# Performance work log

Hardware: AMD Instinct MI355X
Metric: run time of the kernel (lower is better)

## Reference

```python
import jax, jax.numpy as jnp
import numpy as np

U, I, D = 60000, 90000, 64
N = U + I
NNZ_R, NNZ_S = 1_000_000, 1_000_000
N_RATINGS = 5
RATING_LAYERS = 2
SOCIAL_LAYERS = 2
EMB_COMB = 1.0


def setup_inputs() -> dict:
    key = jax.random.key(0)
    ks = jax.random.split(key, 24)
    inp = {
        'rating_rows': jax.random.randint(ks[0], (N_RATINGS, NNZ_R), 0, N, dtype=jnp.int32),
        'rating_cols': jax.random.randint(ks[1], (N_RATINGS, NNZ_R), 0, N, dtype=jnp.int32),
        'rating_vals': jax.random.uniform(ks[2], (N_RATINGS, NNZ_R), dtype=jnp.float32),
        'friend_rows': jax.random.randint(ks[3], (NNZ_S,), 0, U, dtype=jnp.int32),
        'friend_cols': jax.random.randint(ks[4], (NNZ_S,), 0, U, dtype=jnp.int32),
        'friend_vals': jax.random.uniform(ks[5], (NNZ_S,), dtype=jnp.float32),
        'group_rows': jax.random.randint(ks[6], (NNZ_S,), 0, U, dtype=jnp.int32),
        'group_cols': jax.random.randint(ks[7], (NNZ_S,), 0, U, dtype=jnp.int32),
        'group_vals': jax.random.uniform(ks[8], (NNZ_S,), dtype=jnp.float32),
        'rating_user_emb': jax.random.normal(ks[9], (N_RATINGS, U, D), dtype=jnp.float32) * 0.1,
        'rating_item_emb': jax.random.normal(ks[10], (N_RATINGS, I, D), dtype=jnp.float32) * 0.1,
        'friend_emb': jax.random.normal(ks[11], (U, D), dtype=jnp.float32) * 0.1,
        'group_emb': jax.random.normal(ks[12], (U, D), dtype=jnp.float32) * 0.1,
        'user_att_w': jax.random.normal(ks[13], (D,), dtype=jnp.float32) * 0.1,
        'user_att_mat_w': jax.random.normal(ks[14], (D, D), dtype=jnp.float32) * 0.1,
        'item_att_w': jax.random.normal(ks[15], (D,), dtype=jnp.float32) * 0.1,
        'item_att_mat_w': jax.random.normal(ks[16], (D, D), dtype=jnp.float32) * 0.1,
        'social_att_w': jax.random.normal(ks[17], (D,), dtype=jnp.float32) * 0.1,
        'social_att_mat_w': jax.random.normal(ks[18], (D, D), dtype=jnp.float32) * 0.1,
        'adaptive_emb_comb': jax.random.uniform(ks[19], (U,), dtype=jnp.float32) + 0.5,
    }
    return inp


def _spmm(rows, cols, vals, x, n):
    # COO sparse matmul: out[r] += vals[e] * x[cols[e]]
    return jax.ops.segment_sum(vals[:, None] * x[cols], rows, num_segments=n)


def _l2norm(x):
    # F.normalize(x, p=2, dim=1)
    return x / jnp.clip(jnp.linalg.norm(x, axis=1, keepdims=True), 1e-12)


def _att_fuse(embs, a, M):
    # embs: [C, N, D]; weight[c,n] = tanh((emb @ M.T) @ a); softmax over channels C
    w = jnp.tanh(jnp.einsum('cnd,ed,e->cn', embs, M, a))
    scores = jax.nn.softmax(w, axis=0)  # [C, N]
    mixed = jnp.einsum('cn,cnd->nd', scores, embs)
    return mixed, scores


def reference(rating_rows, rating_cols, rating_vals,
              friend_rows, friend_cols, friend_vals,
              group_rows, group_cols, group_vals,
              rating_user_emb, rating_item_emb, friend_emb, group_emb,
              user_att_w, user_att_mat_w, item_att_w, item_att_mat_w,
              social_att_w, social_att_mat_w, adaptive_emb_comb):
    # ---- rating channels: LightGCN propagation over bipartite graph ----
    user_list, item_list = [], []
    for c in range(N_RATINGS):
        ego = jnp.concatenate([rating_user_emb[c], rating_item_emb[c]], axis=0)  # [N, D]
        layers = []
        for _ in range(RATING_LAYERS):
            ego = _spmm(rating_rows[c], rating_cols[c], rating_vals[c], ego, N)
            layers.append(ego)
        mean_emb = jnp.mean(jnp.stack(layers, axis=0), axis=0)
        user_list.append(mean_emb[:U])
        item_list.append(mean_emb[U:])
    user_embs = jnp.stack(user_list, axis=0)  # [C, U, D]
    item_embs = jnp.stack(item_list, axis=0)  # [C, I, D]
    mixed_rating_user, user_scores = _att_fuse(user_embs, user_att_w, user_att_mat_w)
    mixed_rating_item, item_scores = _att_fuse(item_embs, item_att_w, item_att_mat_w)

    # ---- social channels: propagation + per-layer L2 normalize ----
    def social_prop(rows, cols, vals, emb):
        outs = []
        for _ in range(SOCIAL_LAYERS):
            emb = _l2norm(_spmm(rows, cols, vals, emb, U))
            outs.append(emb)
        return jnp.mean(jnp.stack(outs, axis=0), axis=0)

    friend_u = social_prop(friend_rows, friend_cols, friend_vals, friend_emb)
    group_u = social_prop(group_rows, group_cols, group_vals, group_emb)
    social_embs = jnp.stack([friend_u, group_u], axis=0)  # [2, U, D]
    mixed_social, social_scores = _att_fuse(social_embs, social_att_w, social_att_mat_w)

    # ---- adaptive combination ----
    num = jnp.sum(mixed_rating_user * mixed_social, axis=1)
    denom = (jnp.clip(jnp.linalg.norm(mixed_rating_user, axis=1), 1e-8)
             * jnp.clip(jnp.linalg.norm(mixed_social, axis=1), 1e-8))
    emb_sim = num / denom
    emb_sim_up_0 = jnp.maximum(emb_sim, 0.0)
    base = (SOCIAL_LAYERS + RATING_LAYERS) / 2.0
    rate = EMB_COMB / (base + emb_sim_up_0 * adaptive_emb_comb)[:, None]  # [U, 1]
    mixed_user = mixed_rating_user + mixed_social * rate
    return (user_scores, item_scores, social_scores, mixed_user, mixed_rating_item)
```

## Files before the change

### kernel.cpp

```cpp
#include <hip/hip_runtime.h>
#include <hip/hip_bf16.h>

#define UU 60000
#define II 90000
#define DD 64
#define NN 150000
#define NNZC 1000000
#define NTOT 7000000
#define MTOT 870000
#define ROW_S0 750000
#define NBR 733
#define NBCK 1046
#define CAPE 8192
#define ACH 16384
#define GRID_A 428
#define ABLK 1024

__device__ __forceinline__ int wave_incl_scan(int x) {
    int lane = threadIdx.x & 63;
#pragma unroll
    for (int d = 1; d < 64; d <<= 1) {
        int y = __shfl_up(x, d, 64);
        if (lane >= d) x += y;
    }
    return x;
}

__device__ int block_incl_scan(int x, int* lds) {
    int wid = threadIdx.x >> 6, lane = threadIdx.x & 63;
    int ws_ = wave_incl_scan(x);
    if (lane == 63) lds[wid] = ws_;
    __syncthreads();
    int off = 0;
    for (int w = 0; w < wid; ++w) off += lds[w];
    __syncthreads();
    return ws_ + off;
}

__device__ __forceinline__ float2 unpack_bf16x2(unsigned p) {
    float2 r;
    r.x = __uint_as_float(p << 16);
    r.y = __uint_as_float(p & 0xffff0000u);
    return r;
}

__device__ __forceinline__ unsigned pack_bf16x2(float a, float b) {
    __hip_bfloat162 h = __float22bfloat162_rn(make_float2(a, b));
    return *(unsigned*)&h;
}

__device__ __forceinline__ uint2 pack4(float4 m) {
    return make_uint2(pack_bf16x2(m.x, m.y), pack_bf16x2(m.z, m.w));
}

__device__ __forceinline__ float4 unpack4(uint2 p) {
    float2 a = unpack_bf16x2(p.x), b = unpack_bf16x2(p.y);
    return make_float4(a.x, a.y, b.x, b.y);
}

__device__ __forceinline__ int bid_of(int grow) {
    return (grow < ROW_S0) ? (grow >> 10) : NBR + (grow - ROW_S0) / 384;
}

__global__ void att_vec_kernel(const float* __restrict__ au, const float* __restrict__ Mu,
                               const float* __restrict__ ai, const float* __restrict__ Mi,
                               const float* __restrict__ as_, const float* __restrict__ Ms,
                               float* __restrict__ v) {
    int d = threadIdx.x;
    float su = 0.f, si = 0.f, ss = 0.f;
    for (int e = 0; e < DD; ++e) {
        su += au[e] * Mu[e * DD + d];
        si += ai[e] * Mi[e * DD + d];
        ss += as_[e] * Ms[e * DD + d];
    }
    v[d] = su;
    v[DD + d] = si;
    v[2 * DD + d] = ss;
}

__device__ __forceinline__ void decode_full(int e, const int* __restrict__ rR,
                                            const int* __restrict__ rC, const float* __restrict__ rV,
                                            const int* __restrict__ fR, const int* __restrict__ fC,
                                            const float* __restrict__ fV,
                                            const int* __restrict__ gR, const int* __restrict__ gC,
                                            const float* __restrict__ gV,
                                            int& grow, int& c, float& v) {
    if (e < 5 * NNZC) { grow = (e / NNZC) * NN + rR[e]; c = rC[e]; v = rV[e]; }
    else if (e < 6 * NNZC) { int k = e - 5 * NNZC; grow = ROW_S0 + fR[k]; c = fC[k]; v = fV[k]; }
    else { int k = e - 6 * NNZC; grow = ROW_S0 + UU + gR[k]; c = gC[k]; v = gV[k]; }
}

__global__ __launch_bounds__(ABLK) void pa_count_kernel(const int* __restrict__ rR,
                                                        const int* __restrict__ fR,
                                                        const int* __restrict__ gR,
                                                        int* __restrict__ gHistT) {
    __shared__ int lcnt[NBCK];
    int k = blockIdx.x;
    int cbase = k * ACH;
    int eEnd = min(cbase + ACH, NTOT);
    for (int b = threadIdx.x; b < NBCK; b += ABLK) lcnt[b] = 0;
    __syncthreads();
    for (int e0 = cbase + threadIdx.x; e0 < eEnd; e0 += 4 * ABLK) {
        int gw[4]; bool val[4];
#pragma unroll
        for (int u = 0; u < 4; ++u) {
            int e = e0 + u * ABLK;
            val[u] = e < eEnd;
            int ec = val[u] ? e : cbase;
            if (ec < 5 * NNZC) gw[u] = (ec / NNZC) * NN + rR[ec];
            else if (ec < 6 * NNZC) gw[u] = ROW_S0 + fR[ec - 5 * NNZC];
            else gw[u] = ROW_S0 + UU + gR[ec - 6 * NNZC];
        }
#pragma unroll
        for (int u = 0; u < 4; ++u)
            if (val[u]) atomicAdd(&lcnt[bid_of(gw[u])], 1);
    }
    __syncthreads();
    for (int b = threadIdx.x; b < NBCK; b += ABLK)
        gHistT[(size_t)b * GRID_A + k] = lcnt[b];
}

__global__ void kprefix_kernel(int* __restrict__ gHistT, int* __restrict__ bTot) {
    int b = blockIdx.x * (blockDim.x >> 6) + (threadIdx.x >> 6);
    if (b >= NBCK) return;
    int lane = threadIdx.x & 63;
    int* g = gHistT + (size_t)b * GRID_A;
    int carry = 0;
    for (int c0 = 0; c0 < GRID_A; c0 += 64) {
        int idx = c0 + lane;
        int v = (idx < GRID_A) ? g[idx] : 0;
        int incl = wave_incl_scan(v);
        if (idx < GRID_A) g[idx] = carry + incl - v;
        carry += __shfl(incl, 63, 64);
    }
    if (lane == 0) bTot[b] = carry;
}

__global__ void bscan_kernel(const int* __restrict__ bTot, int* __restrict__ bStart,
                             int* __restrict__ rowptr) {
    __shared__ int lds8[8];
    __shared__ int sOff;
    if (threadIdx.x == 0) sOff = 0;
    __syncthreads();
    for (int base = 0; base < NBCK; base += 256) {
        int i = base + threadIdx.x;
        int v = (i < NBCK) ? bTot[i] : 0;
        int incl = block_incl_scan(v, lds8);
        if (i < NBCK) bStart[i] = sOff + incl - v;
        __syncthreads();
        if (threadIdx.x == 255) sOff += incl;
        __syncthreads();
    }
    if (threadIdx.x == 0) { bStart[NBCK] = sOff; rowptr[MTOT] = sOff; }
}

__global__ __launch_bounds__(ABLK) void pa_scatter_kernel(
        const int* __restrict__ rR, const int* __restrict__ rC, const float* __restrict__ rV,
        const int* __restrict__ fR, const int* __restrict__ fC, const float* __restrict__ fV,
        const int* __restrict__ gR, const int* __restrict__ gC, const float* __restrict__ gV,
        const int* __restrict__ bStart, const int* __restrict__ gHistT,
        uint2* __restrict__ ecv) {
    __shared__ int lcur[NBCK];
    int k = blockIdx.x;
    int cbase = k * ACH;
    int eEnd = min(cbase + ACH, NTOT);
    for (int b = threadIdx.x; b < NBCK; b += ABLK)
        lcur[b] = bStart[b] + gHistT[(size_t)b * GRID_A + k];
    __syncthreads();
    for (int e0 = cbase + threadIdx.x; e0 < eEnd; e0 += 4 * ABLK) {
        int gw[4], cc[4]; float vv[4]; bool val[4];
#pragma unroll
        for (int u = 0; u < 4; ++u) {
            int e = e0 + u * ABLK;
            val[u] = e < eEnd;
            int ec = val[u] ? e : cbase;
            decode_full(ec, rR, rC, rV, fR, fC, fV, gR, gC, gV, gw[u], cc[u], vv[u]);
        }
        int pos[4];
#pragma unroll
        for (int u = 0; u < 4; ++u)
            pos[u] = val[u] ? atomicAdd(&lcur[bid_of(gw[u])], 1) : 0;
#pragma unroll
        for (int u = 0; u < 4; ++u) {
            if (!val[u]) continue;
            int lrow = (gw[u] < ROW_S0) ? (gw[u] & 1023) : ((gw[u] - ROW_S0) % 384);
            ecv[pos[u]] = make_uint2(((unsigned)lrow << 18) | (unsigned)cc[u],
                                     __float_as_uint(vv[u]));
        }
    }
}

__global__ __launch_bounds__(256) void phaseB_kernel(const int* __restrict__ bStart,
                                                     int* __restrict__ rowptr,
                                                     const uint2* __restrict__ ecv,
                                                     uint2* __restrict__ edata) {
    __shared__ unsigned short perm[CAPE];
    __shared__ int off[1024];
    __shared__ int lds8[8];
    int b = blockIdx.x;
    int firstRow = (b < NBR) ? (b << 10) : ROW_S0 + (b - NBR) * 384;
    int rowEnd = (b < NBR) ? min((b + 1) << 10, ROW_S0)
                           : min(ROW_S0 + (b - NBR + 1) * 384, MTOT);
    int nRows = rowEnd - firstRow;
    int dst = bStart[b];
    int count = bStart[b + 1] - dst;
    for (int i = threadIdx.x; i < nRows; i += 256) off[i] = 0;
    __syncthreads();
    for (int i = threadIdx.x; i < count; i += 256)
        atomicAdd(&off[ecv[dst + i].x >> 18], 1);
    __syncthreads();
    int base4 = threadIdx.x * 4;
    int v4[4], s = 0;
#pragma unroll
    for (int kk = 0; kk < 4; ++kk) {
        int i = base4 + kk;
        v4[kk] = (i < nRows) ? off[i] : 0;
        s += v4[kk];
    }
    int incl = block_incl_scan(s, lds8);
    int run = incl - s;
#pragma unroll
    for (int kk = 0; kk < 4; ++kk) {
        int i = base4 + kk;
        if (i < nRows) { rowptr[firstRow + i] = dst + run; off[i] = run; }
        run += v4[kk];
    }
    __syncthreads();
    if (count <= CAPE) {
        for (int i = threadIdx.x; i < count; i += 256) {
            int pos = atomicAdd(&off[ecv[dst + i].x >> 18], 1);
            perm[pos] = (unsigned short)i;
        }
        __syncthreads();
        for (int i = threadIdx.x; i < count; i += 256) {
            uint2 e = ecv[dst + perm[i]];
            edata[dst + i] = make_uint2(e.x & 0x3FFFFu, e.y);
        }
    } else {
        for (int i = threadIdx.x; i < count; i += 256) {
            uint2 e = ecv[dst + i];
            int pos = atomicAdd(&off[e.x >> 18], 1);
            edata[dst + pos] = make_uint2(e.x & 0x3FFFFu, e.y);
        }
    }
}

template <int MODE>
__global__ __launch_bounds__(256) void spmm_kernel(
        const int* __restrict__ rowptr, int rowBase,
        const uint2* __restrict__ edata,
        const float* __restrict__ xloF, const float* __restrict__ xhiF,
        const uint2* __restrict__ tblB,
        const uint2* __restrict__ selfB, const float* __restrict__ vvec,
        uint2* __restrict__ outB, float4* __restrict__ outF,
        float* __restrict__ wOut, int nRows) {
    int lane = threadIdx.x & 63;
    int l16 = lane & 15;
    int grpBase = lane & 48;
    int wid = blockIdx.x * (blockDim.x >> 6) + (threadIdx.x >> 6);
    int row = wid * 4 + (lane >> 4);
    bool active = row < nRows;
    int g = rowBase + row;
    int start = active ? rowptr[g] : 0;
    int end = active ? rowptr[g + 1] : 0;
    float4 acc = make_float4(0.f, 0.f, 0.f, 0.f);
    for (int j0 = start; j0 < end; j0 += 16) {
        uint2 md = make_uint2(0u, 0u);
        if (j0 + l16 < end) md = edata[j0 + l16];
        int cnt = min(end - j0, 16);
        for (int js = 0; js < cnt; js += 8) {
            int cc[8]; float vv[8]; float4 xv[8];
#pragma unroll
            for (int u = 0; u < 8; ++u) {
                int jj = js + u;
                int sl = grpBase + ((jj < cnt) ? jj : 0);
                cc[u] = __shfl((int)md.x, sl, 64);
                float v = __uint_as_float((unsigned)__shfl((int)md.y, sl, 64));
                vv[u] = (jj < cnt) ? v : 0.f;
            }
#pragma unroll
            for (int u = 0; u < 8; ++u) {
                int c = cc[u];
                if (MODE == 0) {
                    const float* src = (c < UU) ? (xloF + (size_t)c * DD)
                                                : (xhiF + (size_t)(c - UU) * DD);
                    xv[u] = *(const float4*)(src + 4 * l16);
                } else if (MODE == 2) {
                    xv[u] = *(const float4*)(xloF + (size_t)c * DD + 4 * l16);
                } else {
                    xv[u] = unpack4(tblB[(size_t)c * 16 + l16]);
                }
            }
#pragma unroll
            for (int u = 0; u < 8; ++u) {
                acc.x += vv[u] * xv[u].x; acc.y += vv[u] * xv[u].y;
                acc.z += vv[u] * xv[u].z; acc.w += vv[u] * xv[u].w;
            }
        }
    }
    if (!active) return;
    size_t ro = (size_t)row * 16 + l16;
    if (MODE == 0) {
        outB[ro] = pack4(acc);
    } else if (MODE == 1) {
        float4 sv = unpack4(selfB[ro]);
        float4 m = make_float4(0.5f * (acc.x + sv.x), 0.5f * (acc.y + sv.y),
                               0.5f * (acc.z + sv.z), 0.5f * (acc.w + sv.w));
        outB[ro] = pack4(m);
        const float* vv = (row < UU) ? vvec : (vvec + DD);
        float4 vw = *(const float4*)(vv + 4 * l16);
        float p = m.x * vw.x + m.y * vw.y + m.z * vw.z + m.w * vw.w;
        p += __shfl_xor(p, 1, 64); p += __shfl_xor(p, 2, 64);
        p += __shfl_xor(p, 4, 64); p += __shfl_xor(p, 8, 64);
        if (l16 == 0) wOut[row] = tanhf(p);
    } else if (MODE == 2) {
        float n2 = acc.x * acc.x + acc.y * acc.y + acc.z * acc.z + acc.w * acc.w;
        n2 += __shfl_xor(n2, 1, 64); n2 += __shfl_xor(n2, 2, 64);
        n2 += __shfl_xor(n2, 4, 64); n2 += __shfl_xor(n2, 8, 64);
        float inv = 1.f / fmaxf(sqrtf(n2), 1e-12f);
        outB[ro] = pack4(make_float4(acc.x * inv, acc.y * inv, acc.z * inv, acc.w * inv));
    } else {
        float n2 = acc.x * acc.x + acc.y * acc.y + acc.z * acc.z + acc.w * acc.w;
        n2 += __shfl_xor(n2, 1, 64); n2 += __shfl_xor(n2, 2, 64);
        n2 += __shfl_xor(n2, 4, 64); n2 += __shfl_xor(n2, 8, 64);
        float inv = 1.f / fmaxf(sqrtf(n2), 1e-12f);
        float4 sv = unpack4(selfB[ro]);
        outF[ro] = make_float4(0.5f * (sv.x + acc.x * inv), 0.5f * (sv.y + acc.y * inv),
                               0.5f * (sv.z + acc.z * inv), 0.5f * (sv.w + acc.w * inv));
    }
}

__global__ void mix5_kernel(const __hip_bfloat16* __restrict__ chanEmb,
                            const float* __restrict__ w,
                            float* __restrict__ oUS, float* __restrict__ oIS,
                            float* __restrict__ mixedRU, float* __restrict__ oMI) {
    int lane = threadIdx.x & 63;
    int n = blockIdx.x * (blockDim.x >> 6) + (threadIdx.x >> 6);
    if (n >= NN) return;
    float sw[5];
    float mx = -2.0f;
#pragma unroll
    for (int c = 0; c < 5; ++c) {
        sw[c] = w[(size_t)c * NN + n];
        mx = fmaxf(mx, sw[c]);
    }
    float sum = 0.f;
#pragma unroll
    for (int c = 0; c < 5; ++c) {
        sw[c] = expf(sw[c] - mx);
        sum += sw[c];
    }
    float inv = 1.0f / sum;
    float acc = 0.f;
#pragma unroll
    for (int c = 0; c < 5; ++c) {
        sw[c] *= inv;
        acc += sw[c] * __bfloat162float(chanEmb[((size_t)c * NN + n) * DD + lane]);
    }
    if (n < UU) {
#pragma unroll
        for (int c = 0; c < 5; ++c)
            if (lane == c) oUS[(size_t)c * UU + n] = sw[c];
        mixedRU[(size_t)n * DD + lane] = acc;
    } else {
        int m = n - UU;
#pragma unroll
        for (int c = 0; c < 5; ++c)
            if (lane == c) oIS[(size_t)c * II + m] = sw[c];
        oMI[(size_t)m * DD + lane] = acc;
    }
}

__global__ void social_mix_final_kernel(const float* __restrict__ e0, const float* __restrict__ e1,
                                        const float* __restrict__ vs,
                                        const float* __restrict__ mixedRU,
                                        const float* __restrict__ adaptive,
                                        float* __restrict__ scoresOut,
                                        float* __restrict__ outMU) {
    int lane = threadIdx.x & 63;
    int n = blockIdx.x * (blockDim.x >> 6) + (threadIdx.x >> 6);
    if (n >= UU) return;
    size_t idx = (size_t)n * DD + lane;
    float a = e0[idx];
    float b = e1[idx];
    float v = vs[lane];
    float pa = a * v, pb = b * v;
    float mru = mixedRU[idx];
#pragma unroll
    for (int m = 32; m >= 1; m >>= 1) { pa += __shfl_xor(pa, m, 64); pb += __shfl_xor(pb, m, 64); }
    float w0 = tanhf(pa);
    float w1 = tanhf(pb);
    float mx = fmaxf(w0, w1);
    float x0 = expf(w0 - mx);
    float x1 = expf(w1 - mx);
    float invs = 1.0f / (x0 + x1);
    float s0 = x0 * invs;
    float s1 = x1 * invs;
    if (lane == 0) {
        scoresOut[n] = s0;
        scoresOut[UU + n] = s1;
    }
    float ms = s0 * a + s1 * b;
    float nm = mru * ms, na2 = mru * mru, nb2 = ms * ms;
#pragma unroll
    for (int m = 32; m >= 1; m >>= 1) {
        nm += __shfl_xor(nm, m, 64); na2 += __shfl_xor(na2, m, 64); nb2 += __shfl_xor(nb2, m, 64);
    }
    float denom = fmaxf(sqrtf(na2), 1e-8f) * fmaxf(sqrtf(nb2), 1e-8f);
    float sim = nm / denom;
    float rate = 1.0f / (2.0f + fmaxf(sim, 0.f) * adaptive[n]);
    outMU[idx] = mru + ms * rate;
}

extern "C" void kernel_launch(void* const* d_in, const int* in_sizes, int n_in,
                              void* d_out, int out_size, void* d_ws, size_t ws_size,
                              hipStream_t stream) {
    const int* r_rows = (const int*)d_in[0];
    const int* r_cols = (const int*)d_in[1];
    const float* r_vals = (const float*)d_in[2];
    const int* f_rows = (const int*)d_in[3];
    const int* f_cols = (const int*)d_in[4];
    const float* f_vals = (const float*)d_in[5];
    const int* g_rows = (const int*)d_in[6];
    const int* g_cols = (const int*)d_in[7];
    const float* g_vals = (const float*)d_in[8];
    const float* rue = (const float*)d_in[9];
    const float* rie = (const float*)d_in[10];
    const float* femb = (const float*)d_in[11];
    const float* gemb = (const float*)d_in[12];
    const float* uaw = (const float*)d_in[13];
    const float* uamw = (const float*)d_in[14];
    const float* iaw = (const float*)d_in[15];
    const float* iamw = (const float*)d_in[16];
    const float* saw = (const float*)d_in[17];
    const float* samw = (const float*)d_in[18];
    const float* adapt = (const float*)d_in[19];

    float* ws = (float*)d_ws;
    size_t o = 0;
    int* rowptr = (int*)(ws + o); o += 870016;
    int* bStart = (int*)(ws + o); o += 2048;
    int* bTot   = (int*)(ws + o); o += 2048;
    int* gHistT = (int*)(ws + o); o += 448000;
    float* R1 = ws + o; o += 14000000;
    float* edF = ws + o; o += 14000000;
    float* R2 = ws + o; o += 24000000;
    float* wrat = ws + o; o += 750016;
    float* vvec = ws + o; o += 192;

    uint2* ecv = (uint2*)R1;
    uint2* edata = (uint2*)edF;
    uint2* AtmpB = (uint2*)R1;
    float* mixedRU = R1;
    float* socM0 = R1 + 4800000;
    float* socM1 = R1 + 8640000;
    __hip_bfloat16* chanMean = (__hip_bfloat16*)R2;
    uint2* socL1B = (uint2*)R2;

    float* out = (float*)d_out;
    float* oUS = out;
    float* oIS = oUS + (size_t)5 * UU;
    float* oSS = oIS + (size_t)5 * II;
    float* oMU = oSS + (size_t)2 * UU;
    float* oMI = oMU + (size_t)UU * DD;

    const dim3 blk(256);
    const dim3 blkA(ABLK);
    const int gridN4 = (NN + 15) / 16;
    const int gridU4 = (UU + 15) / 16;
    const int gridMix = (NN + 3) / 4;
    const int gridFin = (UU + 3) / 4;

    att_vec_kernel<<<1, 64, 0, stream>>>(uaw, uamw, iaw, iamw, saw, samw, vvec);

    pa_count_kernel<<<GRID_A, blkA, 0, stream>>>(r_rows, f_rows, g_rows, gHistT);
    kprefix_kernel<<<(NBCK + 3) / 4, blk, 0, stream>>>(gHistT, bTot);
    bscan_kernel<<<1, blk, 0, stream>>>(bTot, bStart, rowptr);
    pa_scatter_kernel<<<GRID_A, blkA, 0, stream>>>(r_rows, r_cols, r_vals,
                                                   f_rows, f_cols, f_vals,
                                                   g_rows, g_cols, g_vals,
                                                   bStart, gHistT, ecv);
    phaseB_kernel<<<NBCK, blk, 0, stream>>>(bStart, rowptr, ecv, edata);

    for (int c = 0; c < 5; ++c) {
        spmm_kernel<0><<<gridN4, blk, 0, stream>>>(
            rowptr, c * NN, edata,
            rue + (size_t)c * UU * DD, rie + (size_t)c * II * DD, nullptr,
            nullptr, nullptr, AtmpB, nullptr, nullptr, NN);
        spmm_kernel<1><<<gridN4, blk, 0, stream>>>(
            rowptr, c * NN, edata,
            nullptr, nullptr, AtmpB, AtmpB, vvec,
            (uint2*)(chanMean + (size_t)c * NN * DD), nullptr, wrat + (size_t)c * NN, NN);
    }

    mix5_kernel<<<gridMix, blk, 0, stream>>>(chanMean, wrat, oUS, oIS, mixedRU, oMI);

    spmm_kernel<2><<<gridU4, blk, 0, stream>>>(rowptr, ROW_S0, edata, femb, nullptr, nullptr,
                                               nullptr, nullptr, socL1B, nullptr, nullptr, UU);
    spmm_kernel<3><<<gridU4, blk, 0, stream>>>(rowptr, ROW_S0, edata, nullptr, nullptr, socL1B,
                                               socL1B, nullptr, nullptr, (float4*)socM0, nullptr, UU);
    spmm_kernel<2><<<gridU4, blk, 0, stream>>>(rowptr, ROW_S0 + UU, edata, gemb, nullptr, nullptr,
                                               nullptr, nullptr, socL1B, nullptr, nullptr, UU);
    spmm_kernel<3><<<gridU4, blk, 0, stream>>>(rowptr, ROW_S0 + UU, edata, nullptr, nullptr, socL1B,
                                               socL1B, nullptr, nullptr, (float4*)socM1, nullptr, UU);

    social_mix_final_kernel<<<gridFin, blk, 0, stream>>>(socM0, socM1, vvec + 2 * DD,
                                                         mixedRU, adapt, oSS, oMU);
}
```

Before: 662.6 us.

## Merge independent SpMM stages into combined launches and precompute scatter ranks

Layer-1 SpMM for channel c now runs in the same launch as layer-2 for channel c-1, with double-buffered intermediates. The first social layers for friend and group are fused into the rating mix kernel, and both second social layers share one launch. The count pass also records each edge's LDS atomic rank, so the scatter pass computes positions without repeating the atomics. This cuts the launch count and raises occupancy for the small kernels. In exchange it adds an extra rank array write and read, larger workspace buffers, and a runtime mode switch in the dual kernel.

```diff
diff --git a/kernel.cpp b/kernel.cpp
--- a/kernel.cpp
+++ b/kernel.cpp
@@ -16,6 +16,19 @@
 #define GRID_A 428
 #define ABLK 1024
 
+struct SpmmJob {
+    int mode;
+    int rowBase;
+    int nRows;
+    const float* xloF;
+    const float* xhiF;
+    const uint2* tblB;
+    const uint2* selfB;
+    uint2* outB;
+    float4* outF;
+    float* wOut;
+};
+
 __device__ __forceinline__ int wave_incl_scan(int x) {
     int lane = threadIdx.x & 63;
 #pragma unroll
@@ -93,7 +106,8 @@
 __global__ __launch_bounds__(ABLK) void pa_count_kernel(const int* __restrict__ rR,
                                                         const int* __restrict__ fR,
                                                         const int* __restrict__ gR,
-                                                        int* __restrict__ gHistT) {
+                                                        int* __restrict__ gHistT,
+                                                        unsigned short* __restrict__ grank) {
     __shared__ int lcnt[NBCK];
     int k = blockIdx.x;
     int cbase = k * ACH;
@@ -111,9 +125,13 @@
             else if (ec < 6 * NNZC) gw[u] = ROW_S0 + fR[ec - 5 * NNZC];
             else gw[u] = ROW_S0 + UU + gR[ec - 6 * NNZC];
         }
+        int rk[4];
 #pragma unroll
         for (int u = 0; u < 4; ++u)
-            if (val[u]) atomicAdd(&lcnt[bid_of(gw[u])], 1);
+            rk[u] = val[u] ? atomicAdd(&lcnt[bid_of(gw[u])], 1) : 0;
+#pragma unroll
+        for (int u = 0; u < 4; ++u)
+            if (val[u]) grank[e0 + u * ABLK] = (unsigned short)rk[u];
     }
     __syncthreads();
     for (int b = threadIdx.x; b < NBCK; b += ABLK)
@@ -159,7 +177,7 @@
         const int* __restrict__ fR, const int* __restrict__ fC, const float* __restrict__ fV,
         const int* __restrict__ gR, const int* __restrict__ gC, const float* __restrict__ gV,
         const int* __restrict__ bStart, const int* __restrict__ gHistT,
-        uint2* __restrict__ ecv) {
+        const unsigned short* __restrict__ grank, uint2* __restrict__ ecv) {
     __shared__ int lcur[NBCK];
     int k = blockIdx.x;
     int cbase = k * ACH;
@@ -168,24 +186,22 @@
         lcur[b] = bStart[b] + gHistT[(size_t)b * GRID_A + k];
     __syncthreads();
     for (int e0 = cbase + threadIdx.x; e0 < eEnd; e0 += 4 * ABLK) {
-        int gw[4], cc[4]; float vv[4]; bool val[4];
+        int gw[4], cc[4]; float vv[4]; int rk[4]; bool val[4];
 #pragma unroll
         for (int u = 0; u < 4; ++u) {
             int e = e0 + u * ABLK;
             val[u] = e < eEnd;
             int ec = val[u] ? e : cbase;
             decode_full(ec, rR, rC, rV, fR, fC, fV, gR, gC, gV, gw[u], cc[u], vv[u]);
-        }
-        int pos[4];
-#pragma unroll
-        for (int u = 0; u < 4; ++u)
-            pos[u] = val[u] ? atomicAdd(&lcur[bid_of(gw[u])], 1) : 0;
+            rk[u] = grank[ec];
+        }
 #pragma unroll
         for (int u = 0; u < 4; ++u) {
             if (!val[u]) continue;
+            int pos = lcur[bid_of(gw[u])] + rk[u];
             int lrow = (gw[u] < ROW_S0) ? (gw[u] & 1023) : ((gw[u] - ROW_S0) % 384);
-            ecv[pos[u]] = make_uint2(((unsigned)lrow << 18) | (unsigned)cc[u],
-                                     __float_as_uint(vv[u]));
+            ecv[pos] = make_uint2(((unsigned)lrow << 18) | (unsigned)cc[u],
+                                  __float_as_uint(vv[u]));
         }
     }
 }
@@ -246,21 +262,17 @@
 }
 
 template <int MODE>
-__global__ __launch_bounds__(256) void spmm_kernel(
-        const int* __restrict__ rowptr, int rowBase,
-        const uint2* __restrict__ edata,
-        const float* __restrict__ xloF, const float* __restrict__ xhiF,
-        const uint2* __restrict__ tblB,
-        const uint2* __restrict__ selfB, const float* __restrict__ vvec,
-        uint2* __restrict__ outB, float4* __restrict__ outF,
-        float* __restrict__ wOut, int nRows) {
+__device__ __forceinline__ void spmm_body(int blk, const SpmmJob& j,
+                                          const int* __restrict__ rowptr,
+                                          const uint2* __restrict__ edata,
+                                          const float* __restrict__ vvec) {
     int lane = threadIdx.x & 63;
     int l16 = lane & 15;
     int grpBase = lane & 48;
-    int wid = blockIdx.x * (blockDim.x >> 6) + (threadIdx.x >> 6);
+    int wid = blk * (int)(blockDim.x >> 6) + (threadIdx.x >> 6);
     int row = wid * 4 + (lane >> 4);
-    bool active = row < nRows;
-    int g = rowBase + row;
+    bool active = row < j.nRows;
+    int g = j.rowBase + row;
     int start = active ? rowptr[g] : 0;
     int end = active ? rowptr[g + 1] : 0;
     float4 acc = make_float4(0.f, 0.f, 0.f, 0.f);
@@ -282,13 +294,13 @@
             for (int u = 0; u < 8; ++u) {
                 int c = cc[u];
                 if (MODE == 0) {
-                    const float* src = (c < UU) ? (xloF + (size_t)c * DD)
-                                                : (xhiF + (size_t)(c - UU) * DD);
+                    const float* src = (c < UU) ? (j.xloF + (size_t)c * DD)
+                                                : (j.xhiF + (size_t)(c - UU) * DD);
                     xv[u] = *(const float4*)(src + 4 * l16);
                 } else if (MODE == 2) {
-                    xv[u] = *(const float4*)(xloF + (size_t)c * DD + 4 * l16);
+                    xv[u] = *(const float4*)(j.xloF + (size_t)c * DD + 4 * l16);
                 } else {
-                    xv[u] = unpack4(tblB[(size_t)c * 16 + l16]);
+                    xv[u] = unpack4(j.tblB[(size_t)c * 16 + l16]);
                 }
             }
 #pragma unroll
@@ -301,41 +313,73 @@
     if (!active) return;
     size_t ro = (size_t)row * 16 + l16;
     if (MODE == 0) {
-        outB[ro] = pack4(acc);
+        j.outB[ro] = pack4(acc);
     } else if (MODE == 1) {
-        float4 sv = unpack4(selfB[ro]);
+        float4 sv = unpack4(j.selfB[ro]);
         float4 m = make_float4(0.5f * (acc.x + sv.x), 0.5f * (acc.y + sv.y),
                                0.5f * (acc.z + sv.z), 0.5f * (acc.w + sv.w));
-        outB[ro] = pack4(m);
+        j.outB[ro] = pack4(m);
         const float* vv = (row < UU) ? vvec : (vvec + DD);
         float4 vw = *(const float4*)(vv + 4 * l16);
         float p = m.x * vw.x + m.y * vw.y + m.z * vw.z + m.w * vw.w;
         p += __shfl_xor(p, 1, 64); p += __shfl_xor(p, 2, 64);
         p += __shfl_xor(p, 4, 64); p += __shfl_xor(p, 8, 64);
-        if (l16 == 0) wOut[row] = tanhf(p);
+        if (l16 == 0) j.wOut[row] = tanhf(p);
     } else if (MODE == 2) {
         float n2 = acc.x * acc.x + acc.y * acc.y + acc.z * acc.z + acc.w * acc.w;
         n2 += __shfl_xor(n2, 1, 64); n2 += __shfl_xor(n2, 2, 64);
         n2 += __shfl_xor(n2, 4, 64); n2 += __shfl_xor(n2, 8, 64);
         float inv = 1.f / fmaxf(sqrtf(n2), 1e-12f);
-        outB[ro] = pack4(make_float4(acc.x * inv, acc.y * inv, acc.z * inv, acc.w * inv));
+        j.outB[ro] = pack4(make_float4(acc.x * inv, acc.y * inv, acc.z * inv, acc.w * inv));
     } else {
         float n2 = acc.x * acc.x + acc.y * acc.y + acc.z * acc.z + acc.w * acc.w;
         n2 += __shfl_xor(n2, 1, 64); n2 += __shfl_xor(n2, 2, 64);
         n2 += __shfl_xor(n2, 4, 64); n2 += __shfl_xor(n2, 8, 64);
         float inv = 1.f / fmaxf(sqrtf(n2), 1e-12f);
-        float4 sv = unpack4(selfB[ro]);
-        outF[ro] = make_float4(0.5f * (sv.x + acc.x * inv), 0.5f * (sv.y + acc.y * inv),
-                               0.5f * (sv.z + acc.z * inv), 0.5f * (sv.w + acc.w * inv));
-    }
-}
-
-__global__ void mix5_kernel(const __hip_bfloat16* __restrict__ chanEmb,
-                            const float* __restrict__ w,
-                            float* __restrict__ oUS, float* __restrict__ oIS,
-                            float* __restrict__ mixedRU, float* __restrict__ oMI) {
+        float4 sv = unpack4(j.selfB[ro]);
+        j.outF[ro] = make_float4(0.5f * (sv.x + acc.x * inv), 0.5f * (sv.y + acc.y * inv),
+                                 0.5f * (sv.z + acc.z * inv), 0.5f * (sv.w + acc.w * inv));
+    }
+}
+
+template <int MODE>
+__global__ __launch_bounds__(256) void spmm_kernel(SpmmJob j, const int* __restrict__ rowptr,
+                                                   const uint2* __restrict__ edata,
+                                                   const float* __restrict__ vvec) {
+    spmm_body<MODE>(blockIdx.x, j, rowptr, edata, vvec);
+}
+
+__global__ __launch_bounds__(256) void spmm_dual_kernel(SpmmJob a, int aBlocks, SpmmJob b,
+                                                        const int* __restrict__ rowptr,
+                                                        const uint2* __restrict__ edata,
+                                                        const float* __restrict__ vvec) {
+    SpmmJob j;
+    int blk;
+    if ((int)blockIdx.x < aBlocks) { j = a; blk = blockIdx.x; }
+    else { j = b; blk = blockIdx.x - aBlocks; }
+    switch (j.mode) {
+        case 0: spmm_body<0>(blk, j, rowptr, edata, vvec); break;
+        case 1: spmm_body<1>(blk, j, rowptr, edata, vvec); break;
+        case 2: spmm_body<2>(blk, j, rowptr, edata, vvec); break;
+        default: spmm_body<3>(blk, j, rowptr, edata, vvec); break;
+    }
+}
+
+__global__ __launch_bounds__(256) void mix_social_kernel(
+        const __hip_bfloat16* __restrict__ chanEmb, const float* __restrict__ w,
+        float* __restrict__ oUS, float* __restrict__ oIS,
+        float* __restrict__ mixedRU, float* __restrict__ oMI, int nMix,
+        SpmmJob s0, int s0Blocks, SpmmJob s1,
+        const int* __restrict__ rowptr, const uint2* __restrict__ edata,
+        const float* __restrict__ vvec) {
+    if ((int)blockIdx.x >= nMix) {
+        int r = blockIdx.x - nMix;
+        if (r < s0Blocks) spmm_body<2>(r, s0, rowptr, edata, vvec);
+        else spmm_body<2>(r - s0Blocks, s1, rowptr, edata, vvec);
+        return;
+    }
     int lane = threadIdx.x & 63;
-    int n = blockIdx.x * (blockDim.x >> 6) + (threadIdx.x >> 6);
+    int n = blockIdx.x * 4 + (threadIdx.x >> 6);
     if (n >= NN) return;
     float sw[5];
     float mx = -2.0f;
@@ -369,6 +413,14 @@
             if (lane == c) oIS[(size_t)c * II + m] = sw[c];
         oMI[(size_t)m * DD + lane] = acc;
     }
+}
+
+__global__ __launch_bounds__(256) void social2_kernel(SpmmJob s0, int s0Blocks, SpmmJob s1,
+                                                      const int* __restrict__ rowptr,
+                                                      const uint2* __restrict__ edata,
+                                                      const float* __restrict__ vvec) {
+    if ((int)blockIdx.x < s0Blocks) spmm_body<3>(blockIdx.x, s0, rowptr, edata, vvec);
+    else spmm_body<3>(blockIdx.x - s0Blocks, s1, rowptr, edata, vvec);
 }
 
 __global__ void social_mix_final_kernel(const float* __restrict__ e0, const float* __restrict__ e1,
@@ -447,15 +499,19 @@
     float* R2 = ws + o; o += 24000000;
     float* wrat = ws + o; o += 750016;
     float* vvec = ws + o; o += 192;
+    float* socF = ws + o; o += 3840000;
 
     uint2* ecv = (uint2*)R1;
     uint2* edata = (uint2*)edF;
-    uint2* AtmpB = (uint2*)R1;
+    unsigned short* grank = (unsigned short*)R2;
+    uint2* AtmpB0 = (uint2*)R1;
+    uint2* AtmpB1 = AtmpB0 + (size_t)NN * 16;
     float* mixedRU = R1;
     float* socM0 = R1 + 4800000;
     float* socM1 = R1 + 8640000;
     __hip_bfloat16* chanMean = (__hip_bfloat16*)R2;
-    uint2* socL1B = (uint2*)R2;
+    uint2* socL1B0 = (uint2*)socF;
+    uint2* socL1B1 = socL1B0 + (size_t)UU * 16;
 
     float* out = (float*)d_out;
     float* oUS = out;
@@ -473,36 +529,51 @@
 
     att_vec_kernel<<<1, 64, 0, stream>>>(uaw, uamw, iaw, iamw, saw, samw, vvec);
 
-    pa_count_kernel<<<GRID_A, blkA, 0, stream>>>(r_rows, f_rows, g_rows, gHistT);
+    pa_count_kernel<<<GRID_A, blkA, 0, stream>>>(r_rows, f_rows, g_rows, gHistT, grank);
     kprefix_kernel<<<(NBCK + 3) / 4, blk, 0, stream>>>(gHistT, bTot);
     bscan_kernel<<<1, blk, 0, stream>>>(bTot, bStart, rowptr);
     pa_scatter_kernel<<<GRID_A, blkA, 0, stream>>>(r_rows, r_cols, r_vals,
                                                    f_rows, f_cols, f_vals,
                                                    g_rows, g_cols, g_vals,
-                                                   bStart, gHistT, ecv);
+                                                   bStart, gHistT, grank, ecv);
     phaseB_kernel<<<NBCK, blk, 0, stream>>>(bStart, rowptr, ecv, edata);
 
-    for (int c = 0; c < 5; ++c) {
-        spmm_kernel<0><<<gridN4, blk, 0, stream>>>(
-            rowptr, c * NN, edata,
-            rue + (size_t)c * UU * DD, rie + (size_t)c * II * DD, nullptr,
-            nullptr, nullptr, AtmpB, nullptr, nullptr, NN);
-        spmm_kernel<1><<<gridN4, blk, 0, stream>>>(
-            rowptr, c * NN, edata,
-            nullptr, nullptr, AtmpB, AtmpB, vvec,
-            (uint2*)(chanMean + (size_t)c * NN * DD), nullptr, wrat + (size_t)c * NN, NN);
-    }
-
-    mix5_kernel<<<gridMix, blk, 0, stream>>>(chanMean, wrat, oUS, oIS, mixedRU, oMI);
-
-    spmm_kernel<2><<<gridU4, blk, 0, stream>>>(rowptr, ROW_S0, edata, femb, nullptr, nullptr,
-                                               nullptr, nullptr, socL1B, nullptr, nullptr, UU);
-    spmm_kernel<3><<<gridU4, blk, 0, stream>>>(rowptr, ROW_S0, edata, nullptr, nullptr, socL1B,
-                                               socL1B, nullptr, nullptr, (float4*)socM0, nullptr, UU);
-    spmm_kernel<2><<<gridU4, blk, 0, stream>>>(rowptr, ROW_S0 + UU, edata, gemb, nullptr, nullptr,
-                                               nullptr, nullptr, socL1B, nullptr, nullptr, UU);
-    spmm_kernel<3><<<gridU4, blk, 0, stream>>>(rowptr, ROW_S0 + UU, edata, nullptr, nullptr, socL1B,
-                                               socL1B, nullptr, nullptr, (float4*)socM1, nullptr, UU);
+    auto jobL1 = [&](int c) {
+        SpmmJob j{};
+        j.mode = 0; j.rowBase = c * NN; j.nRows = NN;
+        j.xloF = rue + (size_t)c * UU * DD;
+        j.xhiF = rie + (size_t)c * II * DD;
+        j.outB = (c & 1) ? AtmpB1 : AtmpB0;
+        return j;
+    };
+    auto jobL2 = [&](int c) {
+        SpmmJob j{};
+        j.mode = 1; j.rowBase = c * NN; j.nRows = NN;
+        j.tblB = (c & 1) ? AtmpB1 : AtmpB0;
+        j.selfB = j.tblB;
+        j.outB = (uint2*)(chanMean + (size_t)c * NN * DD);
+        j.wOut = wrat + (size_t)c * NN;
+        return j;
+    };
+    spmm_kernel<0><<<gridN4, blk, 0, stream>>>(jobL1(0), rowptr, edata, vvec);
+    for (int c = 1; c < 5; ++c)
+        spmm_dual_kernel<<<2 * gridN4, blk, 0, stream>>>(jobL1(c), gridN4, jobL2(c - 1),
+                                                         rowptr, edata, vvec);
+    spmm_kernel<1><<<gridN4, blk, 0, stream>>>(jobL2(4), rowptr, edata, vvec);
+
+    SpmmJob sf1{}; sf1.mode = 2; sf1.rowBase = ROW_S0; sf1.nRows = UU;
+    sf1.xloF = femb; sf1.outB = socL1B0;
+    SpmmJob sg1{}; sg1.mode = 2; sg1.rowBase = ROW_S0 + UU; sg1.nRows = UU;
+    sg1.xloF = gemb; sg1.outB = socL1B1;
+    mix_social_kernel<<<gridMix + 2 * gridU4, blk, 0, stream>>>(
+        chanMean, wrat, oUS, oIS, mixedRU, oMI, gridMix,
+        sf1, gridU4, sg1, rowptr, edata, vvec);
+
+    SpmmJob sf2{}; sf2.mode = 3; sf2.rowBase = ROW_S0; sf2.nRows = UU;
+    sf2.tblB = socL1B0; sf2.selfB = socL1B0; sf2.outF = (float4*)socM0;
+    SpmmJob sg2{}; sg2.mode = 3; sg2.rowBase = ROW_S0 + UU; sg2.nRows = UU;
+    sg2.tblB = socL1B1; sg2.selfB = socL1B1; sg2.outF = (float4*)socM1;
+    social2_kernel<<<2 * gridU4, blk, 0, stream>>>(sf2, gridU4, sg2, rowptr, edata, vvec);
 
     social_mix_final_kernel<<<gridFin, blk, 0, stream>>>(socM0, socM1, vvec + 2 * DD,
                                                          mixedRU, adapt, oSS, oMU);
```

After: 664.6 us. No clear change (+0.3%).
